# Performance work log

Measured on AMD Instinct MI355X. Metric: run time of the kernel, lower is better.

The kernel has to match this reference:

```python
import jax, jax.numpy as jnp
import numpy as np

N = 128            # codeword length (power of 2)
LIST = 8           # SCL list size
L2 = 2 * LIST      # decoders kept during path expansion
STAGES = 7         # log2(N)
LLR_MAX = 30.0
BATCH = 2048
FROZEN_POS = np.arange(N // 2)
FROZEN_IND = np.zeros(N, dtype=bool)
FROZEN_IND[FROZEN_POS] = True
INFO_POS = np.setdiff1d(np.arange(N), FROZEN_POS)


def _cn_op(x, y):
    # min-sum boxplus with LLR clipping
    x = jnp.clip(x, -LLR_MAX, LLR_MAX)
    y = jnp.clip(y, -LLR_MAX, LLR_MAX)
    return jnp.sign(x) * jnp.sign(y) * jnp.minimum(jnp.abs(x), jnp.abs(y))


def _vn_op(x, y, u):
    return (1.0 - 2.0 * u) * x + y


def _leaf(state, i):
    # Update single bit i across all 2L decoders, update path metrics,
    # and for info bits sort + duplicate the best L paths.
    uhat, llr, pm, ptr, bidx = state
    frozen = bool(FROZEN_IND[i])
    if not frozen:
        # set bit=1 for the upper half of decoders (path expansion)
        u_slice = uhat[:, :, 0, i]
        u_slice = u_slice.at[bidx[:, None], ptr[:, LIST:]].set(1.0)
        uhat = uhat.at[:, :, 0, i].set(u_slice)
    # path metric update, Eq.(10) of Stimming et al.
    u = jnp.take_along_axis(uhat[:, :, 0, i], ptr, axis=1)
    l = jnp.clip(jnp.take_along_axis(llr[:, :, 0, i], ptr, axis=1), -LLR_MAX, LLR_MAX)
    pm = pm + jax.nn.softplus(-(1.0 - 2.0 * u) * l)
    if not frozen:
        order = jnp.argsort(pm, axis=-1)
        pm = jnp.take_along_axis(pm, order, axis=1)
        ptr = jnp.take_along_axis(ptr, order, axis=1)
        lo = ptr[:, :LIST]
        up = ptr[:, LIST:]
        uhat = uhat.at[bidx[:, None], up].set(uhat[bidx[:, None], lo])
        llr = llr.at[bidx[:, None], up].set(llr[bidx[:, None], lo])
        pm = pm.at[:, LIST:].set(pm[:, :LIST])
    return (uhat, llr, pm, ptr, bidx)


def _decode(state, start, length):
    # recursive SCL tree traversal over contiguous index block [start, start+length)
    if length == 1:
        return _leaf(state, start)
    s = int(np.log2(length))
    h = length // 2
    uhat, llr, pm, ptr, bidx = state
    lsl = slice(start, start + h)
    rsl = slice(start + h, start + length)
    # f (check-node) update -> left child
    f = _cn_op(llr[:, :, s, lsl], llr[:, :, s, rsl])
    llr = llr.at[:, :, s - 1, lsl].set(f)
    uhat, llr, pm, ptr, bidx = _decode((uhat, llr, pm, ptr, bidx), start, h)
    # g (variable-node) update -> right child
    g = _vn_op(llr[:, :, s, lsl], llr[:, :, s, rsl], uhat[:, :, s - 1, lsl])
    llr = llr.at[:, :, s - 1, rsl].set(g)
    uhat, llr, pm, ptr, bidx = _decode((uhat, llr, pm, ptr, bidx), start + h, h)
    # combine partial sums: left XOR right, right pass-through
    ul = uhat[:, :, s - 1, lsl]
    ur = uhat[:, :, s - 1, rsl]
    ux = ul + ur - 2.0 * ul * ur  # XOR for {0,1} values (differentiable form)
    uhat = uhat.at[:, :, s, start:start + length].set(jnp.concatenate([ux, ur], axis=-1))
    return (uhat, llr, pm, ptr, bidx)


def setup_inputs() -> dict:
    key = jax.random.key(0)
    inputs = 2.0 * jax.random.normal(key, (BATCH, N), dtype=jnp.float32)
    return {"inputs": inputs}


def reference(inputs):
    bs = inputs.shape[0]
    llr_ch = -inputs.astype(jnp.float32)  # logits -> LLR sign convention
    uhat = jnp.zeros((bs, L2, STAGES + 1, N), jnp.float32)
    llr = jnp.zeros((bs, L2, STAGES + 1, N), jnp.float32)
    llr = llr.at[:, :, STAGES, :].set(llr_ch[:, None, :])
    pm = jnp.zeros((bs, L2), jnp.float32)
    pm = pm.at[:, 1:LIST].set(LLR_MAX).at[:, LIST + 1:].set(LLR_MAX)
    ptr = jnp.tile(jnp.arange(L2)[None, :], (bs, 1))
    bidx = jnp.arange(bs)
    uhat, llr, pm, ptr, _ = _decode((uhat, llr, pm, ptr, bidx), 0, N)
    # final sort and de-permutation of the list dimension
    order = jnp.argsort(pm, axis=-1)
    pm = jnp.take_along_axis(pm, order, axis=1)
    ptr = jnp.take_along_axis(ptr, order, axis=1)
    uhat = uhat[bidx[:, None], ptr]
    cand = jnp.argmin(pm, axis=-1)
    c_hat = uhat[bidx, cand, 0, :]       # [bs, n] best codeword estimate
    return c_hat[:, INFO_POS]            # [bs, k] info bits
```

## Files before the change

### kernel.cpp

```cpp
#include <hip/hip_runtime.h>
#include <math.h>

#define LMAX 30.0f
typedef unsigned long long ull;
typedef unsigned int u32;

__device__ __forceinline__ float clip30(float x) { return fminf(fmaxf(x, -LMAX), LMAX); }
__device__ __forceinline__ float cnop(float x, float y) {
    x = clip30(x); y = clip30(y);
    const float m = fminf(fabsf(x), fabsf(y));
    const unsigned sg = (__float_as_uint(x) ^ __float_as_uint(y)) & 0x80000000u;
    return __uint_as_float(__float_as_uint(m) | sg);
}

#define SWZF(x, PAT) __int_as_float(__builtin_amdgcn_ds_swizzle(__float_as_int(x), (PAT)))

template<int CTRL>
__device__ __forceinline__ int dppi(int x) {
    return __builtin_amdgcn_update_dpp(x, x, CTRL, 0xF, 0xF, false);
}
template<int CTRL>
__device__ __forceinline__ float dppf(float x) {
    return __int_as_float(dppi<CTRL>(__float_as_int(x)));
}
#define CTL_XOR8 0x128
#define CTL_XOR2 0x4E
#define CTL_XOR1 0xB1

#if __has_builtin(__builtin_amdgcn_permlane16_swap)
typedef int v2j_ __attribute__((ext_vector_type(2)));
__device__ __forceinline__ int swap16i(int x) {
    v2j_ r = __builtin_amdgcn_permlane16_swap(x, x, false, false);
    return (r[0] != x) ? r[0] : r[1];
}
#else
__device__ __forceinline__ int swap16i(int x) { return __builtin_amdgcn_ds_swizzle(x, 0x401F); }
#endif
__device__ __forceinline__ float swap16f(float x) { return __int_as_float(swap16i(__float_as_int(x))); }

__device__ __forceinline__ float gfb(float v, int a) {
    return __int_as_float(__builtin_amdgcn_ds_bpermute(a, __float_as_int(v)));
}
__device__ __forceinline__ u32 gub(u32 v, int a) {
    return (u32)__builtin_amdgcn_ds_bpermute(a, (int)v);
}

__device__ __forceinline__ u32 enc2(u32 w)  { w ^= (w >> 1) & 0x1u; return w; }
__device__ __forceinline__ u32 enc4(u32 w)  { w ^= (w >> 1) & 0x5u; w ^= (w >> 2) & 0x3u; return w; }
__device__ __forceinline__ u32 enc8(u32 w)  { w ^= (w >> 1) & 0x55u; w ^= (w >> 2) & 0x33u;
                                              w ^= (w >> 4) & 0x0fu; return w; }
__device__ __forceinline__ u32 enc16(u32 w) { w ^= (w >> 1) & 0x5555u; w ^= (w >> 2) & 0x3333u;
                                              w ^= (w >> 4) & 0x0f0fu; w ^= (w >> 8) & 0x00ffu; return w; }
__device__ __forceinline__ u32 enc32(u32 w) { w ^= (w >> 1) & 0x55555555u; w ^= (w >> 2) & 0x33333333u;
                                              w ^= (w >> 4) & 0x0f0f0f0fu; w ^= (w >> 8) & 0x00ff00ffu;
                                              w ^= (w >> 16) & 0x0000ffffu; return w; }

struct Dec {
    float C[32];
    float S5[16], S4[8], S3[4], R2[4], R1[2];
    float pm;
    u32 uhPrev, uhCur;
    int rF;
    int mS5, mS4, mS3;
    int q, pos, gbase, A0, idx0;
    u32 upB;
    bool isUp;
};

__device__ __forceinline__ void f6(Dec& s) {
    #pragma unroll
    for (int k = 0; k < 16; ++k) s.S5[k] = cnop(s.C[k], s.C[k + 16]);
}
__device__ __forceinline__ void g6p(Dec& s) {
    const u32 ub = enc32(s.uhPrev);
    #pragma unroll
    for (int k = 0; k < 16; ++k) {
        const int u = (ub >> (s.q + 2 * k)) & 1;
        s.S5[k] = u ? (s.C[k + 16] - s.C[k]) : (s.C[k + 16] + s.C[k]);
    }
}
__device__ __forceinline__ void f5(Dec& s) {
    #pragma unroll
    for (int k = 0; k < 8; ++k) s.S4[k] = cnop(s.S5[k], s.S5[k + 8]);
}
__device__ __forceinline__ void g5l16(Dec& s) {
    const u32 ub = enc16(s.uhCur & 0xffffu);
    const int am = (s.mS5 | s.gbase) << 2;
    #pragma unroll
    for (int k = 0; k < 8; ++k) {
        const float x = gfb(s.S5[k], am), y = gfb(s.S5[k + 8], am);
        const int u = (ub >> (s.q + 2 * k)) & 1;
        s.S4[k] = u ? (y - x) : (y + x);
    }
    s.mS4 = s.pos;
}
__device__ __forceinline__ void f4(Dec& s) {
    #pragma unroll
    for (int k = 0; k < 4; ++k) s.S3[k] = cnop(s.S4[k], s.S4[k + 4]);
}
template<int L> __device__ __forceinline__ void g4l(Dec& s) {
    const u32 ub = enc8((s.uhCur >> (L - 8)) & 0xffu);
    const int am = (s.mS4 | s.gbase) << 2;
    #pragma unroll
    for (int k = 0; k < 4; ++k) {
        const float x = gfb(s.S4[k], am), y = gfb(s.S4[k + 4], am);
        const int u = (ub >> (s.q + 2 * k)) & 1;
        s.S3[k] = u ? (y - x) : (y + x);
    }
    s.mS3 = s.pos;
}
__device__ __forceinline__ void repl2(Dec& s, float t0, float t1) {
    const float P0 = swap16f(t0), P1 = swap16f(t1);
    s.R2[0] = s.q ? P0 : t0; s.R2[1] = s.q ? t0 : P0;
    s.R2[2] = s.q ? P1 : t1; s.R2[3] = s.q ? t1 : P1;
}
__device__ __forceinline__ void f3r(Dec& s) {
    repl2(s, cnop(s.S3[0], s.S3[2]), cnop(s.S3[1], s.S3[3]));
}
template<int L> __device__ __forceinline__ void g3rl(Dec& s) {
    const u32 ub = enc4((s.uhCur >> (L - 4)) & 0xfu);
    const int am = (s.mS3 | s.gbase) << 2;
    const float x0 = gfb(s.S3[0], am), x1 = gfb(s.S3[1], am);
    const float x2 = gfb(s.S3[2], am), x3 = gfb(s.S3[3], am);
    const int u0 = (ub >> s.q) & 1, u1 = (ub >> (s.q + 2)) & 1;
    repl2(s, u0 ? (x2 - x0) : (x2 + x0), u1 ? (x3 - x1) : (x3 + x1));
}
__device__ __forceinline__ void f2(Dec& s) {
    s.R1[0] = cnop(s.R2[0], s.R2[2]); s.R1[1] = cnop(s.R2[1], s.R2[3]);
}
template<int L> __device__ __forceinline__ void g2l(Dec& s) {
    const u32 ub = enc2((s.uhCur >> (L - 2)) & 3u);
    s.R1[0] = (ub & 1) ? (s.R2[2] - s.R2[0]) : (s.R2[2] + s.R2[0]);
    s.R1[1] = (ub & 2) ? (s.R2[3] - s.R2[1]) : (s.R2[3] + s.R2[1]);
}

template<int L, int CLONEMODE>
__device__ __forceinline__ void leafR(Dec& s, float l0, int h) {
    s.uhCur |= s.upB << L;
    const float l = clip30(l0);
    const float tail = log1pf(expf(-fabsf(l)));
    s.pm += (s.isUp ? fmaxf(l, 0.0f) : fmaxf(-l, 0.0f)) + tail;
    int r = 0;
    {
        const u32 pmB = __float_as_uint(s.pm);
        #pragma unroll
        for (int k = 0; k < 8; ++k) {
            const u32 pmj = (u32)__builtin_amdgcn_ds_bpermute(s.A0 + 4 * k, __float_as_int(s.pm));
            r += ((pmj < pmB) || (pmj == pmB && (s.idx0 + k) < s.pos)) ? 1 : 0;
        }
    }
    r += swap16i(r);
    s.rF = r;
    if constexpr (CLONEMODE != 0) {
        if (CLONEMODE == 1 || h == 0) {
            const ull b0 = __ballot(r == 0), b1 = __ballot(r == 1);
            const ull b2 = __ballot(r == 2), b3 = __ballot(r == 3);
            const ull b4 = __ballot(r == 4), b5 = __ballot(r == 5);
            const ull b6 = __ballot(r == 6), b7 = __ballot(r == 7);
            const ull t0 = (s.pos & 1) ? b1 : b0;
            const ull t1 = (s.pos & 1) ? b3 : b2;
            const ull t2 = (s.pos & 1) ? b5 : b4;
            const ull t3 = (s.pos & 1) ? b7 : b6;
            const ull u0 = (s.pos & 2) ? t1 : t0;
            const ull u1 = (s.pos & 2) ? t3 : t2;
            const ull bb = (s.pos & 4) ? u1 : u0;
            const u32 win = (u32)(bb >> s.gbase) & 0xFFFFu;
            const int ga = (((int)__builtin_ctz(win)) | s.gbase) << 2;
            s.pm = gfb(s.pm, ga);
            s.uhCur = gub(s.uhCur, ga);
            if (h != 0) s.uhPrev = gub(s.uhPrev, ga);
            if constexpr ((L & 1) == 0) {
                s.R1[0] = gfb(s.R1[0], ga); s.R1[1] = gfb(s.R1[1], ga);
            }
            if constexpr ((L & 2) == 0) {
                #pragma unroll
                for (int e = 0; e < 4; ++e) s.R2[e] = gfb(s.R2[e], ga);
            }
            if constexpr ((L & 4) == 0) s.mS3 = __builtin_amdgcn_ds_bpermute(ga, s.mS3);
            if constexpr ((L & 8) == 0) s.mS4 = __builtin_amdgcn_ds_bpermute(ga, s.mS4);
            if constexpr ((L & 16) == 0) s.mS5 = __builtin_amdgcn_ds_bpermute(ga, s.mS5);
        }
    }
}

template<int J> __device__ __forceinline__ void evenL(Dec& s, int h) {
    constexpr int t = __builtin_ctz(J);
    if constexpr (t == 4) { g5l16(s); f4(s); s.mS3 = s.pos; }
    if constexpr (t == 3) { g4l<J>(s); }
    if constexpr (t >= 3) { f3r(s); }
    if constexpr (t == 2) { g3rl<J>(s); }
    if constexpr (t >= 2) { f2(s); }
    if constexpr (t == 1) { g2l<J>(s); }
    const float l0 = cnop(s.R1[0], s.R1[1]);
    leafR<J, 1>(s, l0, h);
}
template<int J> __device__ __forceinline__ void oddL(Dec& s, int h) {
    const int ug = (int)((s.uhCur >> (J - 1)) & 1u);
    const float l0 = ug ? (s.R1[1] - s.R1[0]) : (s.R1[1] + s.R1[0]);
    leafR<J, (J == 31 ? 2 : 1)>(s, l0, h);
}
template<int J> __device__ __forceinline__ void pairs(Dec& s, int h) {
    evenL<J>(s, h);
    oddL<J + 1>(s, h);
    if constexpr (J + 2 <= 30) pairs<J + 2>(s, h);
}

#define RLF(x, J) __uint_as_float((u32)__builtin_amdgcn_readlane(__float_as_int(x), (J)))

__global__ __launch_bounds__(64) void scl_kernel(const float* __restrict__ in,
                                                 float* __restrict__ out) {
    __shared__ float chS[128];
    const int lane = threadIdx.x;
    const int w = lane & 31;
    const int d = lane >> 5;
    const int dbase = lane & 32;

    Dec s;
    s.pos = lane & 15;
    s.q = (lane >> 4) & 1;
    s.gbase = lane & 48;
    s.isUp = (lane & 8) != 0;
    s.upB = (u32)((lane >> 3) & 1);
    s.idx0 = s.q << 3;
    s.A0 = (dbase | (s.q << 3)) << 2;
    s.uhPrev = 0; s.uhCur = 0; s.rF = 0;

    const size_t base = ((size_t)blockIdx.x * 2 + d) * 128;
    const float a1 = -in[base + w],      c1 = -in[base + 64 + w];
    const float a2 = -in[base + 32 + w], c2 = -in[base + 96 + w];
    chS[d * 64 + w] = a1 + c1;
    chS[d * 64 + 32 + w] = a2 + c2;
    __syncthreads();
    #pragma unroll
    for (int k = 0; k < 32; ++k) s.C[k] = chS[d * 64 + s.q + 2 * k];

    float v1 = cnop(a1, c1), v2 = cnop(a2, c2);
    { const float n1 = cnop(v1, v2); v2 = v1 + v2; v1 = n1; }
    { const float o1 = swap16f(v1), o2 = swap16f(v2);
      v1 = (w & 16) ? (o1 + v1) : cnop(v1, o1);
      v2 = (w & 16) ? (o2 + v2) : cnop(v2, o2); }
    { const float o1 = dppf<CTL_XOR8>(v1), o2 = dppf<CTL_XOR8>(v2);
      v1 = (w & 8) ? (o1 + v1) : cnop(v1, o1);
      v2 = (w & 8) ? (o2 + v2) : cnop(v2, o2); }
    { const float o1 = SWZF(v1, 0x101F), o2 = SWZF(v2, 0x101F);
      v1 = (w & 4) ? (o1 + v1) : cnop(v1, o1);
      v2 = (w & 4) ? (o2 + v2) : cnop(v2, o2); }
    { const float o1 = dppf<CTL_XOR2>(v1), o2 = dppf<CTL_XOR2>(v2);
      v1 = (w & 2) ? (o1 + v1) : cnop(v1, o1);
      v2 = (w & 2) ? (o2 + v2) : cnop(v2, o2); }
    { const float o1 = dppf<CTL_XOR1>(v1), o2 = dppf<CTL_XOR1>(v2);
      v1 = (w & 1) ? (o1 + v1) : cnop(v1, o1);
      v2 = (w & 1) ? (o2 + v2) : cnop(v2, o2); }
    const float sp1 = fmaxf(-clip30(v1), 0.0f) + log1pf(expf(-fabsf(clip30(v1))));
    const float sp2 = fmaxf(-clip30(v2), 0.0f) + log1pf(expf(-fabsf(clip30(v2))));

    s.pm = ((s.pos == 0) || (s.pos == 8)) ? 0.0f : LMAX;
    if (lane < 32) {
        #pragma unroll
        for (int j = 0; j < 32; ++j) s.pm += RLF(sp1, j);
        #pragma unroll
        for (int j = 0; j < 32; ++j) s.pm += RLF(sp2, j);
    } else {
        #pragma unroll
        for (int j = 32; j < 64; ++j) s.pm += RLF(sp1, j);
        #pragma unroll
        for (int j = 32; j < 64; ++j) s.pm += RLF(sp2, j);
    }

    #pragma unroll 1
    for (int h = 0; h < 2; ++h) {
        if (h == 0) f6(s); else g6p(s);
        s.mS5 = s.pos;
        f5(s); s.mS4 = s.pos;
        f4(s); s.mS3 = s.pos;
        f3r(s); f2(s);
        { const float l0 = cnop(s.R1[0], s.R1[1]); leafR<0, 1>(s, l0, h); }
        oddL<1>(s, h);
        pairs<2>(s, h);
        if (h == 0) { s.uhPrev = s.uhCur; s.uhCur = 0; }
    }

    const ull m = __ballot(s.rF == 0);
    const int bl = dbase + (int)__builtin_ctz((u32)(m >> dbase));
    const u32 b0 = gub(s.uhPrev, bl << 2);
    const u32 b1 = gub(s.uhCur, bl << 2);
    const size_t ob = ((size_t)blockIdx.x * 2 + d) * 64;
    out[ob + w] = (float)((b0 >> w) & 1u);
    out[ob + 32 + w] = (float)((b1 >> w) & 1u);
}

extern "C" void kernel_launch(void* const* d_in, const int* in_sizes, int n_in,
                              void* d_out, int out_size, void* d_ws, size_t ws_size,
                              hipStream_t stream) {
    (void)n_in; (void)out_size; (void)d_ws; (void)ws_size;
    const float* in = (const float*)d_in[0];
    float* out = (float*)d_out;
    const int batch = in_sizes[0] / 128;
    scl_kernel<<<dim3(batch / 2), dim3(64), 0, stream>>>(in, out);
}
```

Before: 51.89 us.

## Decode one codeword per wave using four lanes per decoder

Measured after the change: 59.33 us. +14.3%, slower.

```diff
diff --git a/kernel.cpp b/kernel.cpp
--- a/kernel.cpp
+++ b/kernel.cpp
@@ -27,6 +27,19 @@
 #define CTL_XOR2 0x4E
 #define CTL_XOR1 0xB1
 
+#if __has_builtin(__builtin_amdgcn_permlane32_swap)
+typedef int v2i_ __attribute__((ext_vector_type(2)));
+__device__ __forceinline__ int swap32i(int x) {
+    v2i_ r = __builtin_amdgcn_permlane32_swap(x, x, false, false);
+    return (r[0] != x) ? r[0] : r[1];
+}
+#else
+__device__ __forceinline__ int swap32i(int x) {
+    int a = x, b = x;
+    asm volatile("v_permlane32_swap_b32 %0, %1" : "+v"(a), "+v"(b));
+    return (a != x) ? a : b;
+}
+#endif
 #if __has_builtin(__builtin_amdgcn_permlane16_swap)
 typedef int v2j_ __attribute__((ext_vector_type(2)));
 __device__ __forceinline__ int swap16i(int x) {
@@ -36,6 +49,7 @@
 #else
 __device__ __forceinline__ int swap16i(int x) { return __builtin_amdgcn_ds_swizzle(x, 0x401F); }
 #endif
+__device__ __forceinline__ float swap32f(float x) { return __int_as_float(swap32i(__float_as_int(x))); }
 __device__ __forceinline__ float swap16f(float x) { return __int_as_float(swap16i(__float_as_int(x))); }
 
 __device__ __forceinline__ float gfb(float v, int a) {
@@ -56,74 +70,76 @@
                                               w ^= (w >> 16) & 0x0000ffffu; return w; }
 
 struct Dec {
-    float C[32];
-    float S5[16], S4[8], S3[4], R2[4], R1[2];
+    float C[16];
+    float S5[8], S4[4], S3[2], R2[4], R1[2];
     float pm;
     u32 uhPrev, uhCur;
     int rF;
     int mS5, mS4, mS3;
-    int q, pos, gbase, A0, idx0;
+    int p, pos, gbase, A0, idx0;
     u32 upB;
     bool isUp;
 };
 
 __device__ __forceinline__ void f6(Dec& s) {
     #pragma unroll
-    for (int k = 0; k < 16; ++k) s.S5[k] = cnop(s.C[k], s.C[k + 16]);
+    for (int k = 0; k < 8; ++k) s.S5[k] = cnop(s.C[k], s.C[k + 8]);
 }
 __device__ __forceinline__ void g6p(Dec& s) {
     const u32 ub = enc32(s.uhPrev);
     #pragma unroll
-    for (int k = 0; k < 16; ++k) {
-        const int u = (ub >> (s.q + 2 * k)) & 1;
-        s.S5[k] = u ? (s.C[k + 16] - s.C[k]) : (s.C[k + 16] + s.C[k]);
+    for (int k = 0; k < 8; ++k) {
+        const int u = (ub >> (s.p + 4 * k)) & 1;
+        s.S5[k] = u ? (s.C[k + 8] - s.C[k]) : (s.C[k + 8] + s.C[k]);
     }
 }
 __device__ __forceinline__ void f5(Dec& s) {
     #pragma unroll
-    for (int k = 0; k < 8; ++k) s.S4[k] = cnop(s.S5[k], s.S5[k + 8]);
+    for (int k = 0; k < 4; ++k) s.S4[k] = cnop(s.S5[k], s.S5[k + 4]);
 }
 __device__ __forceinline__ void g5l16(Dec& s) {
     const u32 ub = enc16(s.uhCur & 0xffffu);
     const int am = (s.mS5 | s.gbase) << 2;
     #pragma unroll
-    for (int k = 0; k < 8; ++k) {
-        const float x = gfb(s.S5[k], am), y = gfb(s.S5[k + 8], am);
-        const int u = (ub >> (s.q + 2 * k)) & 1;
+    for (int k = 0; k < 4; ++k) {
+        const float x = gfb(s.S5[k], am), y = gfb(s.S5[k + 4], am);
+        const int u = (ub >> (s.p + 4 * k)) & 1;
         s.S4[k] = u ? (y - x) : (y + x);
     }
     s.mS4 = s.pos;
 }
 __device__ __forceinline__ void f4(Dec& s) {
-    #pragma unroll
-    for (int k = 0; k < 4; ++k) s.S3[k] = cnop(s.S4[k], s.S4[k + 4]);
+    s.S3[0] = cnop(s.S4[0], s.S4[2]); s.S3[1] = cnop(s.S4[1], s.S4[3]);
 }
 template<int L> __device__ __forceinline__ void g4l(Dec& s) {
     const u32 ub = enc8((s.uhCur >> (L - 8)) & 0xffu);
     const int am = (s.mS4 | s.gbase) << 2;
     #pragma unroll
-    for (int k = 0; k < 4; ++k) {
-        const float x = gfb(s.S4[k], am), y = gfb(s.S4[k + 4], am);
-        const int u = (ub >> (s.q + 2 * k)) & 1;
+    for (int k = 0; k < 2; ++k) {
+        const float x = gfb(s.S4[k], am), y = gfb(s.S4[k + 2], am);
+        const int u = (ub >> (s.p + 4 * k)) & 1;
         s.S3[k] = u ? (y - x) : (y + x);
     }
     s.mS3 = s.pos;
 }
-__device__ __forceinline__ void repl2(Dec& s, float t0, float t1) {
-    const float P0 = swap16f(t0), P1 = swap16f(t1);
-    s.R2[0] = s.q ? P0 : t0; s.R2[1] = s.q ? t0 : P0;
-    s.R2[2] = s.q ? P1 : t1; s.R2[3] = s.q ? t1 : P1;
+__device__ __forceinline__ void repl2(Dec& s, float v0) {
+    const float t1 = swap16f(v0);
+    const float lo = (s.p & 1) ? t1 : v0;
+    const float hi = (s.p & 1) ? v0 : t1;
+    const float lo2 = swap32f(lo);
+    const float hi2 = swap32f(hi);
+    s.R2[0] = (s.p < 2) ? lo : lo2; s.R2[1] = (s.p < 2) ? hi : hi2;
+    s.R2[2] = (s.p < 2) ? lo2 : lo; s.R2[3] = (s.p < 2) ? hi2 : hi;
 }
 __device__ __forceinline__ void f3r(Dec& s) {
-    repl2(s, cnop(s.S3[0], s.S3[2]), cnop(s.S3[1], s.S3[3]));
+    repl2(s, cnop(s.S3[0], s.S3[1]));
 }
 template<int L> __device__ __forceinline__ void g3rl(Dec& s) {
     const u32 ub = enc4((s.uhCur >> (L - 4)) & 0xfu);
     const int am = (s.mS3 | s.gbase) << 2;
     const float x0 = gfb(s.S3[0], am), x1 = gfb(s.S3[1], am);
-    const float x2 = gfb(s.S3[2], am), x3 = gfb(s.S3[3], am);
-    const int u0 = (ub >> s.q) & 1, u1 = (ub >> (s.q + 2)) & 1;
-    repl2(s, u0 ? (x2 - x0) : (x2 + x0), u1 ? (x3 - x1) : (x3 + x1));
+    const int u = (ub >> s.p) & 1;
+    repl2(s, u ? (x1 - x0) : (x1 + x0));
 }
 __device__ __forceinline__ void f2(Dec& s) {
     s.R1[0] = cnop(s.R2[0], s.R2[2]); s.R1[1] = cnop(s.R2[1], s.R2[3]);
@@ -144,11 +160,12 @@
     {
         const u32 pmB = __float_as_uint(s.pm);
         #pragma unroll
-        for (int k = 0; k < 8; ++k) {
+        for (int k = 0; k < 4; ++k) {
             const u32 pmj = (u32)__builtin_amdgcn_ds_bpermute(s.A0 + 4 * k, __float_as_int(s.pm));
             r += ((pmj < pmB) || (pmj == pmB && (s.idx0 + k) < s.pos)) ? 1 : 0;
         }
     }
+    r += swap32i(r);
     r += swap16i(r);
     s.rF = r;
     if constexpr (CLONEMODE != 0) {
@@ -209,63 +226,39 @@
 
 __global__ __launch_bounds__(64) void scl_kernel(const float* __restrict__ in,
                                                  float* __restrict__ out) {
-    __shared__ float chS[128];
+    __shared__ float ch6s[64];
     const int lane = threadIdx.x;
-    const int w = lane & 31;
-    const int d = lane >> 5;
-    const int dbase = lane & 32;
 
     Dec s;
     s.pos = lane & 15;
-    s.q = (lane >> 4) & 1;
+    s.p = lane >> 4;
     s.gbase = lane & 48;
     s.isUp = (lane & 8) != 0;
     s.upB = (u32)((lane >> 3) & 1);
-    s.idx0 = s.q << 3;
-    s.A0 = (dbase | (s.q << 3)) << 2;
+    s.idx0 = s.p << 2;
+    s.A0 = (s.gbase | (s.p << 2)) << 2;
     s.uhPrev = 0; s.uhCur = 0; s.rF = 0;
 
-    const size_t base = ((size_t)blockIdx.x * 2 + d) * 128;
-    const float a1 = -in[base + w],      c1 = -in[base + 64 + w];
-    const float a2 = -in[base + 32 + w], c2 = -in[base + 96 + w];
-    chS[d * 64 + w] = a1 + c1;
-    chS[d * 64 + 32 + w] = a2 + c2;
+    const size_t base = (size_t)blockIdx.x * 128;
+    const float a = -in[base + lane];
+    const float c = -in[base + 64 + lane];
+    ch6s[lane] = a + c;
     __syncthreads();
     #pragma unroll
-    for (int k = 0; k < 32; ++k) s.C[k] = chS[d * 64 + s.q + 2 * k];
-
-    float v1 = cnop(a1, c1), v2 = cnop(a2, c2);
-    { const float n1 = cnop(v1, v2); v2 = v1 + v2; v1 = n1; }
-    { const float o1 = swap16f(v1), o2 = swap16f(v2);
-      v1 = (w & 16) ? (o1 + v1) : cnop(v1, o1);
-      v2 = (w & 16) ? (o2 + v2) : cnop(v2, o2); }
-    { const float o1 = dppf<CTL_XOR8>(v1), o2 = dppf<CTL_XOR8>(v2);
-      v1 = (w & 8) ? (o1 + v1) : cnop(v1, o1);
-      v2 = (w & 8) ? (o2 + v2) : cnop(v2, o2); }
-    { const float o1 = SWZF(v1, 0x101F), o2 = SWZF(v2, 0x101F);
-      v1 = (w & 4) ? (o1 + v1) : cnop(v1, o1);
-      v2 = (w & 4) ? (o2 + v2) : cnop(v2, o2); }
-    { const float o1 = dppf<CTL_XOR2>(v1), o2 = dppf<CTL_XOR2>(v2);
-      v1 = (w & 2) ? (o1 + v1) : cnop(v1, o1);
-      v2 = (w & 2) ? (o2 + v2) : cnop(v2, o2); }
-    { const float o1 = dppf<CTL_XOR1>(v1), o2 = dppf<CTL_XOR1>(v2);
-      v1 = (w & 1) ? (o1 + v1) : cnop(v1, o1);
-      v2 = (w & 1) ? (o2 + v2) : cnop(v2, o2); }
-    const float sp1 = fmaxf(-clip30(v1), 0.0f) + log1pf(expf(-fabsf(clip30(v1))));
-    const float sp2 = fmaxf(-clip30(v2), 0.0f) + log1pf(expf(-fabsf(clip30(v2))));
+    for (int k = 0; k < 16; ++k) s.C[k] = ch6s[s.p + 4 * k];
+
+    float v = cnop(a, c);
+    { const float o = swap32f(v);            v = (lane & 32) ? (o + v) : cnop(v, o); }
+    { const float o = swap16f(v);            v = (lane & 16) ? (o + v) : cnop(v, o); }
+    { const float o = dppf<CTL_XOR8>(v);     v = (lane & 8)  ? (o + v) : cnop(v, o); }
+    { const float o = SWZF(v, 0x101F);       v = (lane & 4)  ? (o + v) : cnop(v, o); }
+    { const float o = dppf<CTL_XOR2>(v);     v = (lane & 2)  ? (o + v) : cnop(v, o); }
+    { const float o = dppf<CTL_XOR1>(v);     v = (lane & 1)  ? (o + v) : cnop(v, o); }
+    const float spf = fmaxf(-clip30(v), 0.0f) + log1pf(expf(-fabsf(clip30(v))));
 
     s.pm = ((s.pos == 0) || (s.pos == 8)) ? 0.0f : LMAX;
-    if (lane < 32) {
-        #pragma unroll
-        for (int j = 0; j < 32; ++j) s.pm += RLF(sp1, j);
-        #pragma unroll
-        for (int j = 0; j < 32; ++j) s.pm += RLF(sp2, j);
-    } else {
-        #pragma unroll
-        for (int j = 32; j < 64; ++j) s.pm += RLF(sp1, j);
-        #pragma unroll
-        for (int j = 32; j < 64; ++j) s.pm += RLF(sp2, j);
-    }
+    #pragma unroll
+    for (int j = 0; j < 64; ++j) s.pm += RLF(spf, j);
 
     #pragma unroll 1
     for (int h = 0; h < 2; ++h) {
@@ -281,12 +274,11 @@
     }
 
     const ull m = __ballot(s.rF == 0);
-    const int bl = dbase + (int)__builtin_ctz((u32)(m >> dbase));
-    const u32 b0 = gub(s.uhPrev, bl << 2);
-    const u32 b1 = gub(s.uhCur, bl << 2);
-    const size_t ob = ((size_t)blockIdx.x * 2 + d) * 64;
-    out[ob + w] = (float)((b0 >> w) & 1u);
-    out[ob + 32 + w] = (float)((b1 >> w) & 1u);
+    const int bl = (int)__builtin_ctzll(m);
+    const u32 b0 = (u32)__builtin_amdgcn_readlane((int)s.uhPrev, bl);
+    const u32 b1 = (u32)__builtin_amdgcn_readlane((int)s.uhCur, bl);
+    const u32 bits = (lane < 32) ? b0 : b1;
+    out[(size_t)blockIdx.x * 64 + lane] = (float)((bits >> (lane & 31)) & 1u);
 }
 
 extern "C" void kernel_launch(void* const* d_in, const int* in_sizes, int n_in,
@@ -296,5 +288,5 @@
     const float* in = (const float*)d_in[0];
     float* out = (float*)d_out;
     const int batch = in_sizes[0] / 128;
-    scl_kernel<<<dim3(batch / 2), dim3(64), 0, stream>>>(in, out);
-}
+    scl_kernel<<<dim3(batch), dim3(64), 0, stream>>>(in, out);
+}
```
